# Kernel optimization log

Measured on AMD Instinct MI355X. Metric: run time of the kernel, lower is better.

Reference implementation:

```python
import jax, jax.numpy as jnp
import numpy as np

B, N, M = 2, 2048, 2048
D = 1024          # query_dim == context_dim == inner_dim
H, DH = 16, 64    # heads, dim_head
SCALE = DH ** -0.5


def setup_inputs() -> dict:
    key = jax.random.key(0)
    ks = jax.random.split(key, 7)
    s = 0.02
    return {
        "x": jax.random.normal(ks[0], (B, N, D), jnp.float32),
        "context": jax.random.normal(ks[1], (B, M, D), jnp.float32),
        "Wq": jax.random.normal(ks[2], (D, H * DH), jnp.float32) * s,
        "Wk": jax.random.normal(ks[3], (D, H * DH), jnp.float32) * s,
        "Wv": jax.random.normal(ks[4], (D, H * DH), jnp.float32) * s,
        "Wo": jax.random.normal(ks[5], (H * DH, D), jnp.float32) * s,
        "bo": jax.random.normal(ks[6], (D,), jnp.float32) * s,
    }


def reference(x, context, Wq, Wk, Wv, Wo, bo):
    # Linear projections (bias-free, as in to_q/to_k/to_v)
    q = (x @ Wq).reshape(B, N, H, DH)        # [B,N,H,DH]
    k = (context @ Wk).reshape(B, M, H, DH)  # [B,M,H,DH]
    v = (context @ Wv).reshape(B, M, H, DH)
    # QK^T * scale, softmax over keys, then AV
    sim = jnp.einsum('bnhd,bmhd->bhnm', q, k) * SCALE  # [B,H,N,M]
    attn = jax.nn.softmax(sim, axis=-1)
    out = jnp.einsum('bhnm,bmhd->bnhd', attn, v)       # [B,N,H,DH]
    out = out.reshape(B, N, H * DH)
    return out @ Wo + bo  # to_out Linear; dropout=0 is identity
```

## Files before the change

kernel.cpp:

```cpp
#include <hip/hip_runtime.h>

#define B_  2
#define N_  2048
#define M_  2048
#define D_  1024
#define H_  16
#define DH_ 64

typedef __bf16 bf16x8 __attribute__((ext_vector_type(8)));
typedef __bf16 bf16x4 __attribute__((ext_vector_type(4)));
typedef short  short4v __attribute__((ext_vector_type(4)));
typedef float  f32x4  __attribute__((ext_vector_type(4)));

#define GAS(p) ((__attribute__((address_space(1))) void*)(p))
#define LAS(p) ((__attribute__((address_space(3))) void*)(p))

#define QPRESCALE 0.18033688011112042f

__device__ __forceinline__ unsigned short f2bf(float f) {
    unsigned int u = __builtin_bit_cast(unsigned int, f);
    u += 0x7fffu + ((u >> 16) & 1u);
    return (unsigned short)(u >> 16);
}

__global__ __launch_bounds__(256) void prep(
    const float* __restrict__ x, const float* __restrict__ ctx,
    const float* __restrict__ Wq, const float* __restrict__ Wk,
    const float* __restrict__ Wv, const float* __restrict__ Wo,
    unsigned short* __restrict__ xb, unsigned short* __restrict__ cb,
    unsigned short* __restrict__ WTbase)
{
    if (blockIdx.z == 4) {
        int blk = blockIdx.y * 32 + blockIdx.x;
        int stride = 1024 * 256;
        for (int i = blk * 256 + threadIdx.x; i < 2097152; i += stride) {
            const float4* src; unsigned short* dst; int j;
            if (i < 1048576) { src = (const float4*)x;   dst = xb; j = i; }
            else             { src = (const float4*)ctx; dst = cb; j = i - 1048576; }
            float4 v = src[j];
            ushort4 o = make_ushort4(f2bf(v.x), f2bf(v.y), f2bf(v.z), f2bf(v.w));
            *(ushort4*)(dst + 4*j) = o;
        }
        return;
    }
    const float* W = (blockIdx.z == 0) ? Wq : (blockIdx.z == 1) ? Wk
                    : (blockIdx.z == 2) ? Wv : Wo;
    unsigned short* WT = WTbase + (size_t)blockIdx.z * 1048576;
    __shared__ unsigned short t[32][33];
    int tx = threadIdx.x & 31, ty8 = threadIdx.x >> 5;
    int c = blockIdx.x * 32 + tx;
#pragma unroll
    for (int i = 0; i < 4; ++i) {
        int r = blockIdx.y * 32 + i*8 + ty8;
        t[i*8 + ty8][tx] = f2bf(W[(size_t)r * 1024 + c]);
    }
    __syncthreads();
    int c2 = blockIdx.y * 32 + tx;
#pragma unroll
    for (int i = 0; i < 4; ++i) {
        int r2 = blockIdx.x * 32 + i*8 + ty8;
        WT[(size_t)r2 * 1024 + c2] = t[tx][i*8 + ty8];
    }
}

__global__ __launch_bounds__(256) void gemm128(
    const unsigned short* __restrict__ xb,
    const unsigned short* __restrict__ cb,
    const unsigned short* __restrict__ wT,
    const unsigned short* __restrict__ aoA,
    unsigned short* __restrict__ qkv_out,
    const float* __restrict__ bo,
    float* __restrict__ outF,
    int base_mode)
{
    __shared__ __align__(16) unsigned short As[128*32];
    __shared__ __align__(16) unsigned short Bs[128*32];

    const int mode = base_mode + blockIdx.z;
    const unsigned short* Amat = (mode == 0) ? xb : (mode == 3) ? aoA : cb;
    const unsigned short* Bt = wT + (size_t)mode * 1048576;

    const int tid = threadIdx.x;
    const int w = tid >> 6, l = tid & 63;
    const int quad = l >> 4, l16 = l & 15;
    const int wm = w & 1, wn = w >> 1;
    const int row0 = blockIdx.y * 128, col0 = blockIdx.x * 128;

    f32x4 acc[4][4];
#pragma unroll
    for (int i = 0; i < 4; ++i)
#pragma unroll
        for (int j = 0; j < 4; ++j) acc[i][j] = (f32x4){0.f, 0.f, 0.f, 0.f};

    for (int k0 = 0; k0 < 1024; k0 += 32) {
        __syncthreads();
#pragma unroll
        for (int i = 0; i < 2; ++i) {
            int s = i*256 + w*64 + l;
            int m = s >> 2, c = s & 3;
            int cs = c ^ ((m >> 1) & 3);
            __builtin_amdgcn_global_load_lds(
                GAS(Amat + (size_t)(row0 + m)*1024 + k0 + cs*8),
                LAS(As + (i*256 + w*64)*8), 16, 0, 0);
            __builtin_amdgcn_global_load_lds(
                GAS(Bt + (size_t)(col0 + m)*1024 + k0 + cs*8),
                LAS(Bs + (i*256 + w*64)*8), 16, 0, 0);
        }
        __syncthreads();

        bf16x8 af[4], bfr[4];
#pragma unroll
        for (int mt = 0; mt < 4; ++mt) {
            int m = wm*64 + mt*16 + l16;
            af[mt] = *reinterpret_cast<const bf16x8*>(As + m*32 + (quad ^ ((m >> 1) & 3))*8);
            int n = wn*64 + mt*16 + l16;
            bfr[mt] = *reinterpret_cast<const bf16x8*>(Bs + n*32 + (quad ^ ((n >> 1) & 3))*8);
        }
#pragma unroll
        for (int mt = 0; mt < 4; ++mt)
#pragma unroll
            for (int nt = 0; nt < 4; ++nt)
                acc[mt][nt] = __builtin_amdgcn_mfma_f32_16x16x32_bf16(
                    af[mt], bfr[nt], acc[mt][nt], 0, 0, 0);
    }

    if (mode == 3) {
#pragma unroll
        for (int nt = 0; nt < 4; ++nt) {
            int col = col0 + wn*64 + nt*16 + l16;
            float bv = bo[col];
#pragma unroll
            for (int mt = 0; mt < 4; ++mt) {
                int gr = row0 + wm*64 + mt*16 + quad*4;
#pragma unroll
                for (int r = 0; r < 4; ++r)
                    outF[(size_t)(gr + r)*1024 + col] = acc[mt][nt][r] + bv;
            }
        }
    } else if (mode == 2) {
#pragma unroll
        for (int mt = 0; mt < 4; ++mt) {
            int gr = row0 + wm*64 + mt*16 + quad*4;
            int b = gr >> 11, nidx = gr & 2047;
#pragma unroll
            for (int nt = 0; nt < 4; ++nt) {
                int col = col0 + wn*64 + nt*16 + l16;
                int h = col >> 6, d = col & 63;
                ushort4 pk = make_ushort4(f2bf(acc[mt][nt][0]), f2bf(acc[mt][nt][1]),
                                          f2bf(acc[mt][nt][2]), f2bf(acc[mt][nt][3]));
                *(ushort4*)(qkv_out + (size_t)2*4194304
                            + (size_t)((b*16 + h)*64 + d)*2048 + nidx) = pk;
            }
        }
    } else {
        const float qs = (mode == 0) ? QPRESCALE : 1.0f;
#pragma unroll
        for (int mt = 0; mt < 4; ++mt) {
            int gr = row0 + wm*64 + mt*16 + quad*4;
#pragma unroll
            for (int nt = 0; nt < 4; ++nt) {
                int col = col0 + wn*64 + nt*16 + l16;
                int h = col >> 6, d = col & 63;
#pragma unroll
                for (int r = 0; r < 4; ++r) {
                    int grr = gr + r;
                    int b = grr >> 11, nidx = grr & 2047;
                    qkv_out[(size_t)mode*4194304
                            + (size_t)((b*16 + h)*2048 + nidx)*64 + d]
                        = f2bf(acc[mt][nt][r] * qs);
                }
            }
        }
    }
}

__global__ __launch_bounds__(256, 2) void flash_attn(
    const unsigned short* __restrict__ qw,
    const unsigned short* __restrict__ kw,
    const unsigned short* __restrict__ vtw,
    unsigned short* __restrict__ ao)
{
    __shared__ __align__(16) unsigned short Ks[128*72];
    __shared__ __align__(16) unsigned short Vs[80*136];

    const int tid = threadIdx.x;
    const int w = tid >> 6, l = tid & 63;
    const int quad = l >> 4, l16 = l & 15;
    const int bh = blockIdx.z * H_ + blockIdx.y;
    const int q0 = blockIdx.x * 128 + w * 32;

    {
        const unsigned int ONE2 = 0x3F803F80u;
        uint4* p = (uint4*)(Vs + 8704);
        p[tid] = make_uint4(ONE2, ONE2, ONE2, ONE2);
        if (tid < 16) p[256 + tid] = make_uint4(ONE2, ONE2, ONE2, ONE2);
    }

    int koff[5], voff[5];
#pragma unroll
    for (int i = 0; i < 5; ++i) {
        int n = i*256 + w*64 + l;
        int kv = n / 9, ck = n % 9;  if (ck > 7)  ck = 7;
        koff[i] = kv*64 + ck*8;
        int d  = n / 17, cv = n % 17; if (cv > 15) cv = 15;
        voff[i] = d*2048 + cv*8;
    }
    const int kact4 = (w < 2), vact4 = (w < 1);

    bf16x8 qf[2][2];
#pragma unroll
    for (int qg = 0; qg < 2; ++qg)
#pragma unroll
        for (int s = 0; s < 2; ++s)
            qf[qg][s] = *reinterpret_cast<const bf16x8*>(
                qw + (size_t)(bh*2048 + q0 + qg*16 + l16)*64 + s*32 + quad*8);

    f32x4 accO[2][5];
#pragma unroll
    for (int qg = 0; qg < 2; ++qg)
#pragma unroll
        for (int td = 0; td < 5; ++td) accO[qg][td] = (f32x4){0.f, 0.f, 0.f, 0.f};

    const f32x4 zz = (f32x4){0.f, 0.f, 0.f, 0.f};

    for (int kv0 = 0; kv0 < M_; kv0 += 128) {
        const unsigned short* kp = kw + (size_t)bh*131072 + kv0*64;
        const unsigned short* vp = vtw + (size_t)bh*131072 + kv0;
        __syncthreads();
#pragma unroll
        for (int i = 0; i < 4; ++i)
            __builtin_amdgcn_global_load_lds(GAS(kp + koff[i]),
                LAS(Ks + (i*256 + w*64)*8), 16, 0, 0);
        if (kact4)
            __builtin_amdgcn_global_load_lds(GAS(kp + koff[4]),
                LAS(Ks + (1024 + w*64)*8), 16, 0, 0);
#pragma unroll
        for (int i = 0; i < 4; ++i)
            __builtin_amdgcn_global_load_lds(GAS(vp + voff[i]),
                LAS(Vs + (i*256 + w*64)*8), 16, 0, 0);
        if (vact4)
            __builtin_amdgcn_global_load_lds(GAS(vp + voff[4]),
                LAS(Vs + (1024 + w*64)*8), 16, 0, 0);
        __syncthreads();

        f32x4 sac[2][8];
#pragma unroll
        for (int t = 0; t < 8; ++t) {
            const unsigned short* krow = Ks + (t*16 + l16)*72 + quad*8;
            bf16x8 kf0 = *reinterpret_cast<const bf16x8*>(krow);
            bf16x8 kf1 = *reinterpret_cast<const bf16x8*>(krow + 32);
            sac[0][t] = __builtin_amdgcn_mfma_f32_16x16x32_bf16(kf0, qf[0][0], zz, 0, 0, 0);
            sac[1][t] = __builtin_amdgcn_mfma_f32_16x16x32_bf16(kf0, qf[1][0], zz, 0, 0, 0);
            sac[0][t] = __builtin_amdgcn_mfma_f32_16x16x32_bf16(kf1, qf[0][1], sac[0][t], 0, 0, 0);
            sac[1][t] = __builtin_amdgcn_mfma_f32_16x16x32_bf16(kf1, qf[1][1], sac[1][t], 0, 0, 0);
        }

        short4v pk[2][8];
#pragma unroll
        for (int qg = 0; qg < 2; ++qg)
#pragma unroll
            for (int t = 0; t < 8; ++t) {
                bf16x4 pb;
#pragma unroll
                for (int r = 0; r < 4; ++r)
                    pb[r] = (__bf16)__builtin_amdgcn_exp2f(sac[qg][t][r]);
                pk[qg][t] = __builtin_bit_cast(short4v, pb);
            }

#pragma unroll
        for (int td = 0; td < 5; ++td) {
            const unsigned short* vrow = Vs + (td*16 + l16)*136 + quad*4;
#pragma unroll
            for (int t = 0; t < 8; ++t) {
                short4v vf = *reinterpret_cast<const short4v*>(vrow + t*16);
                accO[0][td] = __builtin_amdgcn_mfma_f32_16x16x16bf16_1k(
                    vf, pk[0][t], accO[0][td], 0, 0, 0);
                accO[1][td] = __builtin_amdgcn_mfma_f32_16x16x16bf16_1k(
                    vf, pk[1][t], accO[1][td], 0, 0, 0);
            }
        }
    }

#pragma unroll
    for (int qg = 0; qg < 2; ++qg) {
        float inv = 1.f / accO[qg][4][0];
        const size_t rowbase =
            (size_t)(blockIdx.z*2048 + q0 + qg*16 + l16)*1024 + blockIdx.y*64;
#pragma unroll
        for (int td = 0; td < 4; ++td)
#pragma unroll
            for (int r = 0; r < 4; ++r)
                ao[rowbase + td*16 + quad*4 + r] = f2bf(accO[qg][td][r] * inv);
    }
}

extern "C" void kernel_launch(void* const* d_in, const int* in_sizes, int n_in,
                              void* d_out, int out_size, void* d_ws, size_t ws_size,
                              hipStream_t stream)
{
    const float* x   = (const float*)d_in[0];
    const float* ctx = (const float*)d_in[1];
    const float* Wq  = (const float*)d_in[2];
    const float* Wk  = (const float*)d_in[3];
    const float* Wv  = (const float*)d_in[4];
    const float* Wo  = (const float*)d_in[5];
    const float* bo  = (const float*)d_in[6];
    float* out = (float*)d_out;

    unsigned short* ws  = (unsigned short*)d_ws;
    unsigned short* xb  = ws;
    unsigned short* cb  = ws + 4194304;
    unsigned short* wT  = ws + 8388608;
    unsigned short* qkv = ws + 12582912;
    unsigned short* ao  = ws;

    prep<<<dim3(32, 32, 5), dim3(256), 0, stream>>>(x, ctx, Wq, Wk, Wv, Wo, xb, cb, wT);
    gemm128<<<dim3(8, 32, 3), dim3(256), 0, stream>>>(xb, cb, wT, ao, qkv, bo, out, 0);
    flash_attn<<<dim3(16, 16, 2), dim3(256), 0, stream>>>(qkv, qkv + 4194304, qkv + 8388608, ao);
    gemm128<<<dim3(8, 32, 1), dim3(256), 0, stream>>>(xb, cb, wT, ao, qkv, bo, out, 3);
}
```

Measured before the change: 224.3 us.

## Double-buffer K/V tiles and compute softmax denominator via register sums

Replaces the single-buffered 128-key K/V tiles with double-buffered 64-key tiles in one shared array, so the next tile's global-to-LDS loads are issued before computing on the current tile. The row-sum trick, which used a ones-padded V block and a fifth MFMA column tile, is replaced by summing the exp2 values in fp32 registers and reducing across lanes with shuffles at the end. The aim is to hide load latency and drop the extra MFMA work. In exchange it runs twice as many iterations with smaller tiles, and the denominator is now summed from fp32 values rather than the bf16-rounded ones used in the numerator.

After: 222.6 us. Within noise of the previous version (-0.8%).

```diff
diff --git a/kernel.cpp b/kernel.cpp
--- a/kernel.cpp
+++ b/kernel.cpp
@@ -180,8 +180,7 @@
     const unsigned short* __restrict__ vtw,
     unsigned short* __restrict__ ao)
 {
-    __shared__ __align__(16) unsigned short Ks[128*72];
-    __shared__ __align__(16) unsigned short Vs[80*136];
+    __shared__ __align__(16) unsigned short Tile[2][9216];
 
     const int tid = threadIdx.x;
     const int w = tid >> 6, l = tid & 63;
@@ -189,23 +188,16 @@
     const int bh = blockIdx.z * H_ + blockIdx.y;
     const int q0 = blockIdx.x * 128 + w * 32;
 
-    {
-        const unsigned int ONE2 = 0x3F803F80u;
-        uint4* p = (uint4*)(Vs + 8704);
-        p[tid] = make_uint4(ONE2, ONE2, ONE2, ONE2);
-        if (tid < 16) p[256 + tid] = make_uint4(ONE2, ONE2, ONE2, ONE2);
-    }
-
-    int koff[5], voff[5];
+    int goff[5];
 #pragma unroll
     for (int i = 0; i < 5; ++i) {
         int n = i*256 + w*64 + l;
-        int kv = n / 9, ck = n % 9;  if (ck > 7)  ck = 7;
-        koff[i] = kv*64 + ck*8;
-        int d  = n / 17, cv = n % 17; if (cv > 15) cv = 15;
-        voff[i] = d*2048 + cv*8;
-    }
-    const int kact4 = (w < 2), vact4 = (w < 1);
+        int m = (n < 576) ? n : n - 576;
+        int row = m / 9, c = m % 9;  if (c > 7) c = 7;
+        goff[i] = (n < 576) ? row*64 + c*8 : row*2048 + c*8;
+    }
+    const unsigned short* kbase = kw + (size_t)bh*131072;
+    const unsigned short* vbase = vtw + (size_t)bh*131072;
 
     bf16x8 qf[2][2];
 #pragma unroll
@@ -215,37 +207,51 @@
             qf[qg][s] = *reinterpret_cast<const bf16x8*>(
                 qw + (size_t)(bh*2048 + q0 + qg*16 + l16)*64 + s*32 + quad*8);
 
-    f32x4 accO[2][5];
+    f32x4 accO[2][4];
 #pragma unroll
     for (int qg = 0; qg < 2; ++qg)
 #pragma unroll
-        for (int td = 0; td < 5; ++td) accO[qg][td] = (f32x4){0.f, 0.f, 0.f, 0.f};
+        for (int td = 0; td < 4; ++td) accO[qg][td] = (f32x4){0.f, 0.f, 0.f, 0.f};
+    float lpart[2] = {0.f, 0.f};
 
     const f32x4 zz = (f32x4){0.f, 0.f, 0.f, 0.f};
 
-    for (int kv0 = 0; kv0 < M_; kv0 += 128) {
-        const unsigned short* kp = kw + (size_t)bh*131072 + kv0*64;
-        const unsigned short* vp = vtw + (size_t)bh*131072 + kv0;
+    {
+#pragma unroll
+        for (int i = 0; i < 4; ++i) {
+            const unsigned short* bp = (i*4 + w < 9) ? kbase : vbase;
+            __builtin_amdgcn_global_load_lds(GAS(bp + goff[i]),
+                LAS(&Tile[0][(i*256 + w*64)*8]), 16, 0, 0);
+        }
+        if (w < 2)
+            __builtin_amdgcn_global_load_lds(GAS(vbase + goff[4]),
+                LAS(&Tile[0][(1024 + w*64)*8]), 16, 0, 0);
+    }
+
+    for (int it = 0; it < 32; ++it) {
         __syncthreads();
-#pragma unroll
-        for (int i = 0; i < 4; ++i)
-            __builtin_amdgcn_global_load_lds(GAS(kp + koff[i]),
-                LAS(Ks + (i*256 + w*64)*8), 16, 0, 0);
-        if (kact4)
-            __builtin_amdgcn_global_load_lds(GAS(kp + koff[4]),
-                LAS(Ks + (1024 + w*64)*8), 16, 0, 0);
-#pragma unroll
-        for (int i = 0; i < 4; ++i)
-            __builtin_amdgcn_global_load_lds(GAS(vp + voff[i]),
-                LAS(Vs + (i*256 + w*64)*8), 16, 0, 0);
-        if (vact4)
-            __builtin_amdgcn_global_load_lds(GAS(vp + voff[4]),
-                LAS(Vs + (1024 + w*64)*8), 16, 0, 0);
-        __syncthreads();
-
-        f32x4 sac[2][8];
-#pragma unroll
-        for (int t = 0; t < 8; ++t) {
+        const int cur = it & 1;
+
+        if (it + 1 < 32) {
+            const unsigned short* kp = kbase + (it+1)*4096;
+            const unsigned short* vp = vbase + (it+1)*64;
+#pragma unroll
+            for (int i = 0; i < 4; ++i) {
+                const unsigned short* bp = (i*4 + w < 9) ? kp : vp;
+                __builtin_amdgcn_global_load_lds(GAS(bp + goff[i]),
+                    LAS(&Tile[cur^1][(i*256 + w*64)*8]), 16, 0, 0);
+            }
+            if (w < 2)
+                __builtin_amdgcn_global_load_lds(GAS(vp + goff[4]),
+                    LAS(&Tile[cur^1][(1024 + w*64)*8]), 16, 0, 0);
+        }
+
+        const unsigned short* Ks = &Tile[cur][0];
+        const unsigned short* Vs = &Tile[cur][4608];
+
+        f32x4 sac[2][4];
+#pragma unroll
+        for (int t = 0; t < 4; ++t) {
             const unsigned short* krow = Ks + (t*16 + l16)*72 + quad*8;
             bf16x8 kf0 = *reinterpret_cast<const bf16x8*>(krow);
             bf16x8 kf1 = *reinterpret_cast<const bf16x8*>(krow + 32);
@@ -255,23 +261,30 @@
             sac[1][t] = __builtin_amdgcn_mfma_f32_16x16x32_bf16(kf1, qf[1][1], sac[1][t], 0, 0, 0);
         }
 
-        short4v pk[2][8];
-#pragma unroll
-        for (int qg = 0; qg < 2; ++qg)
-#pragma unroll
-            for (int t = 0; t < 8; ++t) {
+        short4v pk[2][4];
+#pragma unroll
+        for (int qg = 0; qg < 2; ++qg) {
+            float s0 = 0.f, s1 = 0.f, s2 = 0.f, s3 = 0.f;
+#pragma unroll
+            for (int t = 0; t < 4; ++t) {
+                float p0 = __builtin_amdgcn_exp2f(sac[qg][t][0]);
+                float p1 = __builtin_amdgcn_exp2f(sac[qg][t][1]);
+                float p2 = __builtin_amdgcn_exp2f(sac[qg][t][2]);
+                float p3 = __builtin_amdgcn_exp2f(sac[qg][t][3]);
+                s0 += p0; s1 += p1; s2 += p2; s3 += p3;
                 bf16x4 pb;
-#pragma unroll
-                for (int r = 0; r < 4; ++r)
-                    pb[r] = (__bf16)__builtin_amdgcn_exp2f(sac[qg][t][r]);
+                pb[0] = (__bf16)p0; pb[1] = (__bf16)p1;
+                pb[2] = (__bf16)p2; pb[3] = (__bf16)p3;
                 pk[qg][t] = __builtin_bit_cast(short4v, pb);
             }
-
-#pragma unroll
-        for (int td = 0; td < 5; ++td) {
-            const unsigned short* vrow = Vs + (td*16 + l16)*136 + quad*4;
-#pragma unroll
-            for (int t = 0; t < 8; ++t) {
+            lpart[qg] += (s0 + s1) + (s2 + s3);
+        }
+
+#pragma unroll
+        for (int td = 0; td < 4; ++td) {
+            const unsigned short* vrow = Vs + (td*16 + l16)*72 + quad*4;
+#pragma unroll
+            for (int t = 0; t < 4; ++t) {
                 short4v vf = *reinterpret_cast<const short4v*>(vrow + t*16);
                 accO[0][td] = __builtin_amdgcn_mfma_f32_16x16x16bf16_1k(
                     vf, pk[0][t], accO[0][td], 0, 0, 0);
@@ -283,7 +296,10 @@
 
 #pragma unroll
     for (int qg = 0; qg < 2; ++qg) {
-        float inv = 1.f / accO[qg][4][0];
+        float s = lpart[qg];
+        s += __shfl_xor(s, 16);
+        s += __shfl_xor(s, 32);
+        float inv = 1.f / s;
         const size_t rowbase =
             (size_t)(blockIdx.z*2048 + q0 + qg*16 + l16)*1024 + blockIdx.y*64;
 #pragma unroll
```
